# Performance work log

Hardware: AMD Instinct MI355X
Metric: run time of the kernel (lower is better)

The kernel has to match this reference:

```python
import jax, jax.numpy as jnp
import numpy as np

B, L, H = 16, 512, 1024
K_START, K_END = 5, 5
LN_EPS = 1e-12
NEG = 1e30


def _layer_norm(x, gamma, beta):
    mu = jnp.mean(x, axis=-1, keepdims=True)
    var = jnp.mean(jnp.square(x - mu), axis=-1, keepdims=True)
    return (x - mu) * jax.lax.rsqrt(var + LN_EPS) * gamma + beta


def setup_inputs() -> dict:
    key = jax.random.key(0)
    ks = jax.random.split(key, 10)
    s = 0.02
    sequence_data = jax.random.normal(ks[0], (B, L, H), jnp.float32)
    class_index = jax.random.randint(ks[1], (B,), 0, L, dtype=jnp.int32)
    paragraph_mask = (jax.random.uniform(ks[2], (B, L)) > 0.1).astype(jnp.float32)
    paragraph_mask = paragraph_mask.at[:, 0].set(1.0)  # guarantee >=1 valid position per row
    return {
        'sequence_data': sequence_data,
        'class_index': class_index,
        'paragraph_mask': paragraph_mask,
        'W_start': jax.random.normal(ks[3], (H, 1), jnp.float32) * s,
        'b_start': jnp.zeros((1,), jnp.float32),
        'W_end_in': jax.random.normal(ks[4], (2 * H, H), jnp.float32) * s,
        'b_end_in': jnp.zeros((H,), jnp.float32),
        'ln_gamma': jnp.ones((H,), jnp.float32),
        'ln_beta': jnp.zeros((H,), jnp.float32),
        'W_end_out': jax.random.normal(ks[5], (H, 1), jnp.float32) * s,
        'b_end_out': jnp.zeros((1,), jnp.float32),
        'W_ans_in': jax.random.normal(ks[6], (2 * H, H), jnp.float32) * s,
        'b_ans_in': jnp.zeros((H,), jnp.float32),
        'W_ans_out': jax.random.normal(ks[7], (H, 1), jnp.float32) * s,
    }


def reference(sequence_data, class_index, paragraph_mask,
              W_start, b_start, W_end_in, b_end_in, ln_gamma, ln_beta,
              W_end_out, b_end_out, W_ans_in, b_ans_in, W_ans_out):
    mask = paragraph_mask  # [b, l] float, 1 = valid

    # ---- start logits ----
    start_logits = jnp.einsum('blh,ho->bl', sequence_data, W_start) + b_start[0]  # [b,l]
    masked_start_logits = start_logits * mask - NEG * (1.0 - mask)
    start_predictions = jax.nn.log_softmax(masked_start_logits, axis=-1)

    # ---- beam search over start positions (inference branch) ----
    start_top_predictions, start_top_index = jax.lax.top_k(start_predictions, K_START)  # [b,k]
    # one-hot einsum gather 'blh,bkl->bkh' expressed as direct indexing
    start_features = jnp.take_along_axis(sequence_data, start_top_index[:, :, None], axis=1)  # [b,k,h]

    # end_logits inner dense on concat([tiled seq, tiled start_features]) along h:
    # split the [2h, h] kernel and broadcast-add instead of materializing the tiled concat.
    W1, W2 = W_end_in[:H], W_end_in[H:]
    inner = jnp.tanh(
        jnp.einsum('blh,hd->bld', sequence_data, W1)[:, :, None, :]
        + jnp.einsum('bkh,hd->bkd', start_features, W2)[:, None, :, :]
        + b_end_in
    )  # [b,l,k,h]
    inner = _layer_norm(inner, ln_gamma, ln_beta)
    end_logits = jnp.einsum('blkh,ho->blk', inner, W_end_out) + b_end_out[0]  # [b,l,k]
    end_logits = jnp.transpose(end_logits, (0, 2, 1))  # [b,k,l]

    mask_k = mask[:, None, :]  # [b,1,l]
    masked_end_logits = end_logits * mask_k - NEG * (1.0 - mask_k)
    end_predictions = jax.nn.log_softmax(masked_end_logits, axis=-1)

    end_top_predictions, _end_top_index = jax.lax.top_k(end_predictions, K_END)  # [b,k,k2]
    end_top_predictions = end_top_predictions.reshape(-1, K_START * K_END)

    # ---- answer (class) logits ----
    class_feature = sequence_data[jnp.arange(sequence_data.shape[0]), class_index]  # [b,h]
    start_p = jax.nn.softmax(masked_start_logits, axis=-1)
    start_feature = jnp.einsum('blh,bl->bh', sequence_data, start_p)
    answer_feature = jnp.concatenate([start_feature, class_feature], axis=-1)  # [b,2h]
    answer_feature = jnp.tanh(answer_feature @ W_ans_in + b_ans_in)  # dropout is identity at inference
    class_logits = (answer_feature @ W_ans_out)[:, 0]  # [b]

    return (start_predictions, end_predictions, masked_start_logits, masked_end_logits,
            start_top_predictions, end_top_predictions, class_logits)
```

## Files before the change

kernel.cpp:

```cpp
#include <hip/hip_runtime.h>
#include <math.h>

#define HD   1024
#define LSEQ 512
#define NB   16
#define KTOP 5
#define NEGV 1e30f

typedef __bf16 bf16x8 __attribute__((ext_vector_type(8)));
typedef float  f32x4  __attribute__((ext_vector_type(4)));

__device__ inline unsigned short f2bf(float f) {
  unsigned u = __float_as_uint(f);
  unsigned r = (u + 0x7FFFu + ((u >> 16) & 1u)) >> 16;
  return (unsigned short)r;
}
__device__ inline float bf2f(unsigned short u) {
  return __uint_as_float(((unsigned)u) << 16);
}

__device__ inline float fast_tanh(float x) {
  float e = __expf(-2.f * fabsf(x));
  float v = (1.f - e) / (1.f + e);
  return copysignf(v, x);
}

__device__ inline float tanh_scaled(float xs) {
  float e = __builtin_amdgcn_exp2f(xs);
  float r = __builtin_amdgcn_rcpf(1.f + e);
  return fmaf(-2.f, r, 1.f);
}

#define GLDS(g, l) __builtin_amdgcn_global_load_lds(                      \
    (const __attribute__((address_space(1))) unsigned int*)(g),          \
    (__attribute__((address_space(3))) unsigned int*)(l), 16, 0, 0)


__device__ __forceinline__ void sm_body(int row, const float* __restrict__ xin,
                                        float* __restrict__ lsm_out,
                                        float* __restrict__ top_out,
                                        float* __restrict__ p_out,
                                        int* __restrict__ idx_out) {
  __shared__ float redf[4];
  __shared__ int redi[4];
  __shared__ float bc_m, bc_s;
  __shared__ int bc_i;
  int t = threadIdx.x, lane = t & 63, wid = t >> 6;
  const float* x = xin + (size_t)row * LSEQ;
  float x0 = x[t], x1 = x[t + 256];

  float m = fmaxf(x0, x1);
#pragma unroll
  for (int off = 32; off; off >>= 1) m = fmaxf(m, __shfl_xor(m, off));
  if (lane == 0) redf[wid] = m;
  __syncthreads();
  if (t == 0) bc_m = fmaxf(fmaxf(redf[0], redf[1]), fmaxf(redf[2], redf[3]));
  __syncthreads();
  m = bc_m;

  float e0 = expf(x0 - m), e1 = expf(x1 - m);
  float s = e0 + e1;
#pragma unroll
  for (int off = 32; off; off >>= 1) s += __shfl_xor(s, off);
  if (lane == 0) redf[wid] = s;
  __syncthreads();
  if (t == 0) bc_s = redf[0] + redf[1] + redf[2] + redf[3];
  __syncthreads();
  s = bc_s;
  float ls = logf(s);

  lsm_out[(size_t)row * LSEQ + t] = x0 - m - ls;
  lsm_out[(size_t)row * LSEQ + t + 256] = x1 - m - ls;
  if (p_out) {
    float inv = 1.f / s;
    p_out[(size_t)row * LSEQ + t] = e0 * inv;
    p_out[(size_t)row * LSEQ + t + 256] = e1 * inv;
  }

  bool a0 = true, a1 = true;
  for (int it = 0; it < KTOP; ++it) {
    float v0 = a0 ? x0 : -INFINITY;
    float v1 = a1 ? x1 : -INFINITY;
    float bv = v0; int bi = t;
    if (v1 > bv) { bv = v1; bi = t + 256; }
#pragma unroll
    for (int off = 32; off; off >>= 1) {
      float ov = __shfl_xor(bv, off);
      int oi = __shfl_xor(bi, off);
      if (ov > bv || (ov == bv && oi < bi)) { bv = ov; bi = oi; }
    }
    __syncthreads();
    if (lane == 0) { redf[wid] = bv; redi[wid] = bi; }
    __syncthreads();
    if (t == 0) {
      float wv = redf[0]; int wi = redi[0];
      for (int w = 1; w < 4; ++w)
        if (redf[w] > wv || (redf[w] == wv && redi[w] < wi)) { wv = redf[w]; wi = redi[w]; }
      top_out[row * KTOP + it] = wv - m - ls;
      if (idx_out) idx_out[row * KTOP + it] = wi;
      bc_i = wi;
    }
    __syncthreads();
    int wi = bc_i;
    if (wi == t) a0 = false;
    if (wi == t + 256) a1 = false;
  }
}

__device__ __forceinline__ void gemm_body(int R0, int C0,
                                          const unsigned short* __restrict__ Abf,
                                          const unsigned short* __restrict__ Bt,
                                          unsigned short* __restrict__ X1) {
  __shared__ unsigned short SH[32768];
  unsigned short* As = SH;
  unsigned short* Bs = SH + 16384;
  int t = threadIdx.x;
  int w = t >> 6, lane = t & 63, ln = lane & 15, hi = lane >> 4;
  int wr = w >> 1, wc = w & 1;

  f32x4 acc[4][4] = {};

#define STAGE(buf, kc)                                                        \
  do {                                                                        \
    _Pragma("unroll")                                                         \
    for (int p_ = 0; p_ < 4; ++p_) {                                          \
      int rr_ = p_ * 32 + (t >> 3);                                           \
      int cc_ = (t & 7) ^ (rr_ & 7);                                          \
      GLDS(Abf + (size_t)(R0 + rr_) * HD + (kc) + cc_ * 8,                    \
           As + (buf) * 8192 + p_ * 2048 + w * 512);                          \
      GLDS(Bt + (size_t)(C0 + rr_) * HD + (kc) + cc_ * 8,                     \
           Bs + (buf) * 8192 + p_ * 2048 + w * 512);                          \
    }                                                                         \
  } while (0)

  STAGE(0, 0);
  for (int it = 0; it < 16; ++it) {
    int cur = it & 1;
    if (it < 15) {
      STAGE(cur ^ 1, (it + 1) * 64);
      asm volatile("s_waitcnt vmcnt(8)" ::: "memory");
    } else {
      asm volatile("s_waitcnt vmcnt(0)" ::: "memory");
    }
    __builtin_amdgcn_s_barrier();
    __builtin_amdgcn_sched_barrier(0);
#pragma unroll
    for (int ks = 0; ks < 2; ++ks) {
      bf16x8 av[4], bv[4];
#pragma unroll
      for (int m = 0; m < 4; ++m) {
        int r = wr * 64 + m * 16 + ln;
        av[m] = *(const bf16x8*)(const void*)&As[cur * 8192 + r * 64 + (((ks * 4 + hi) ^ (r & 7)) * 8)];
      }
#pragma unroll
      for (int n = 0; n < 4; ++n) {
        int r = wc * 64 + n * 16 + ln;
        bv[n] = *(const bf16x8*)(const void*)&Bs[cur * 8192 + r * 64 + (((ks * 4 + hi) ^ (r & 7)) * 8)];
      }
#pragma unroll
      for (int m = 0; m < 4; ++m)
#pragma unroll
        for (int n = 0; n < 4; ++n)
          acc[m][n] = __builtin_amdgcn_mfma_f32_16x16x32_bf16(av[m], bv[n], acc[m][n], 0, 0, 0);
    }
    __builtin_amdgcn_sched_barrier(0);
    __builtin_amdgcn_s_barrier();
  }
#undef STAGE

#pragma unroll
  for (int m = 0; m < 4; ++m)
#pragma unroll
    for (int j = 0; j < 4; ++j) {
      int row = R0 + wr * 64 + m * 16 + hi * 4 + j;
#pragma unroll
      for (int n = 0; n < 4; ++n) {
        int col = C0 + wc * 64 + n * 16 + ln;
        X1[(size_t)row * HD + col] = f2bf(acc[m][n][j]);
      }
    }
}

__device__ __forceinline__ void x2gemm_body(int cid,
                                            const unsigned short* __restrict__ seqb,
                                            const unsigned short* __restrict__ w2t,
                                            const int* __restrict__ idx,
                                            const float* __restrict__ bei,
                                            float* __restrict__ x2p) {
  __shared__ unsigned short SH2[32768];
  unsigned short* As = SH2;
  unsigned short* Bs = SH2 + 16384;
  int t = threadIdx.x;
  int w = t >> 6, lane = t & 63, ln = lane & 15, hi = lane >> 4;
  int wr = w >> 1, wc = w & 1;
  int C0 = cid * 128;

  size_t abase[4];
#pragma unroll
  for (int p_ = 0; p_ < 4; ++p_) {
    int rr = p_ * 32 + (t >> 3);
    int bk = rr < 80 ? rr : 0;
    int l = idx[bk];
    abase[p_] = ((size_t)((bk / KTOP) * LSEQ + l)) * HD;
  }

  f32x4 acc[4][4] = {};

#define STAGE2(buf, kc)                                                       \
  do {                                                                        \
    _Pragma("unroll")                                                         \
    for (int p_ = 0; p_ < 4; ++p_) {                                          \
      int rr_ = p_ * 32 + (t >> 3);                                           \
      int cc_ = (t & 7) ^ (rr_ & 7);                                          \
      GLDS(seqb + abase[p_] + (kc) + cc_ * 8,                                 \
           As + (buf) * 8192 + p_ * 2048 + w * 512);                          \
      GLDS(w2t + (size_t)(C0 + rr_) * HD + (kc) + cc_ * 8,                    \
           Bs + (buf) * 8192 + p_ * 2048 + w * 512);                          \
    }                                                                         \
  } while (0)

  STAGE2(0, 0);
  for (int it = 0; it < 16; ++it) {
    int cur = it & 1;
    if (it < 15) {
      STAGE2(cur ^ 1, (it + 1) * 64);
      asm volatile("s_waitcnt vmcnt(8)" ::: "memory");
    } else {
      asm volatile("s_waitcnt vmcnt(0)" ::: "memory");
    }
    __builtin_amdgcn_s_barrier();
    __builtin_amdgcn_sched_barrier(0);
#pragma unroll
    for (int ks = 0; ks < 2; ++ks) {
      bf16x8 av[4], bv[4];
#pragma unroll
      for (int m = 0; m < 4; ++m) {
        int r = wr * 64 + m * 16 + ln;
        av[m] = *(const bf16x8*)(const void*)&As[cur * 8192 + r * 64 + (((ks * 4 + hi) ^ (r & 7)) * 8)];
      }
#pragma unroll
      for (int n = 0; n < 4; ++n) {
        int r = wc * 64 + n * 16 + ln;
        bv[n] = *(const bf16x8*)(const void*)&Bs[cur * 8192 + r * 64 + (((ks * 4 + hi) ^ (r & 7)) * 8)];
      }
#pragma unroll
      for (int m = 0; m < 4; ++m)
#pragma unroll
        for (int n = 0; n < 4; ++n)
          acc[m][n] = __builtin_amdgcn_mfma_f32_16x16x32_bf16(av[m], bv[n], acc[m][n], 0, 0, 0);
    }
    __builtin_amdgcn_sched_barrier(0);
    __builtin_amdgcn_s_barrier();
  }
#undef STAGE2

#pragma unroll
  for (int m = 0; m < 4; ++m)
#pragma unroll
    for (int j = 0; j < 4; ++j) {
      int row = wr * 64 + m * 16 + hi * 4 + j;
      if (row < 80) {
#pragma unroll
        for (int n = 0; n < 4; ++n) {
          int col = C0 + wc * 64 + n * 16 + ln;
          x2p[(size_t)row * HD + col] = acc[m][n][j] + bei[col];
        }
      }
    }
}

__device__ __forceinline__ void ansin_body(int q, const float* __restrict__ seq,
                                           const float* __restrict__ p_ws,
                                           const int* __restrict__ cls,
                                           float* __restrict__ pa,
                                           float* __restrict__ cf) {
  __shared__ float ps[16];
  int b = q >> 5, s = q & 31, t = threadIdx.x;
  if (t < 16) ps[t] = p_ws[b * LSEQ + s * 16 + t];
  __syncthreads();
  const float* sb = seq + (size_t)(b * LSEQ + s * 16) * HD;
  float4 acc = make_float4(0.f, 0.f, 0.f, 0.f);
#pragma unroll
  for (int r = 0; r < 16; ++r) {
    float4 v = *(const float4*)(sb + (size_t)r * HD + 4 * t);
    float p = ps[r];
    acc.x = fmaf(p, v.x, acc.x);
    acc.y = fmaf(p, v.y, acc.y);
    acc.z = fmaf(p, v.z, acc.z);
    acc.w = fmaf(p, v.w, acc.w);
  }
  *(float4*)(pa + ((size_t)b * 32 + s) * HD + 4 * t) = acc;
  if (s == 0) {
    int ci = cls[b];
    *(float4*)(cf + (size_t)b * HD + 4 * t) =
        *(const float4*)(seq + (size_t)(b * LSEQ + ci) * HD + 4 * t);
  }
}

__device__ __forceinline__ void endrow_body(int bx, const unsigned short* __restrict__ X1,
                                            const float* __restrict__ x2p,
                                            const float* __restrict__ gw_ws,
                                            const float* __restrict__ sgb_ws,
                                            const float* __restrict__ mask,
                                            float* __restrict__ mel) {
  __shared__ float x2s[KTOP * HD];
  const float A = 2.885390081777927f;
  int t = threadIdx.x, wave = t >> 6, lane = t & 63;
  int row = bx * 4 + wave;
  int b = row >> 9, l = row & 511;

  {
    const float4* src = (const float4*)(x2p + (size_t)b * KTOP * HD);
    float4* dst = (float4*)x2s;
    for (int i = t; i < KTOP * HD / 4; i += 256) {
      float4 v = src[i];
      dst[i] = make_float4(v.x * A, v.y * A, v.z * A, v.w * A);
    }
  }

  float xs[16], gwr[16];
  const unsigned short* xrow = X1 + (size_t)row * HD + lane * 4;
#pragma unroll
  for (int q = 0; q < 4; ++q) {
    ushort4 u = *(const ushort4*)(xrow + q * 256);
    xs[4 * q + 0] = bf2f(u.x) * A;
    xs[4 * q + 1] = bf2f(u.y) * A;
    xs[4 * q + 2] = bf2f(u.z) * A;
    xs[4 * q + 3] = bf2f(u.w) * A;
    float4 g = *(const float4*)(gw_ws + q * 256 + lane * 4);
    gwr[4 * q + 0] = g.x; gwr[4 * q + 1] = g.y;
    gwr[4 * q + 2] = g.z; gwr[4 * q + 3] = g.w;
  }
  float mv = mask[row];
  float sG = sgb_ws[0], sBW = sgb_ws[1];
  __syncthreads();

#pragma unroll
  for (int k = 0; k < KTOP; ++k) {
    float sv = 0.f, s2 = 0.f, sg = 0.f;
#pragma unroll
    for (int q = 0; q < 4; ++q) {
      float4 xq = *(const float4*)&x2s[k * HD + q * 256 + lane * 4];
      float v0 = tanh_scaled(xs[4 * q + 0] + xq.x);
      float v1 = tanh_scaled(xs[4 * q + 1] + xq.y);
      float v2 = tanh_scaled(xs[4 * q + 2] + xq.z);
      float v3 = tanh_scaled(xs[4 * q + 3] + xq.w);
      sv += v0 + v1 + v2 + v3;
      s2 = fmaf(v0, v0, s2); s2 = fmaf(v1, v1, s2);
      s2 = fmaf(v2, v2, s2); s2 = fmaf(v3, v3, s2);
      sg = fmaf(v0, gwr[4 * q + 0], sg); sg = fmaf(v1, gwr[4 * q + 1], sg);
      sg = fmaf(v2, gwr[4 * q + 2], sg); sg = fmaf(v3, gwr[4 * q + 3], sg);
    }
#pragma unroll
    for (int off = 32; off; off >>= 1) {
      sv += __shfl_xor(sv, off);
      s2 += __shfl_xor(s2, off);
      sg += __shfl_xor(sg, off);
    }
    if (lane == 0) {
      float mu = sv * (1.f / (float)HD);
      float var = s2 * (1.f / (float)HD) - mu * mu;
      float rr = rsqrtf(var + 1e-12f);
      float logit = rr * (sg - mu * sG) + sBW;
      mel[((size_t)b * KTOP + k) * LSEQ + l] = logit * mv - NEGV * (1.f - mv);
    }
  }
}

__device__ __forceinline__ void ansmid_body(int q, const float* __restrict__ pa,
                                            const float* __restrict__ cf,
                                            const float* __restrict__ Wai,
                                            float* __restrict__ pans) {
  __shared__ float a_s[128];
  int b = q >> 4, c = q & 15, t = threadIdx.x;
  if (t < 128) {
    int i = c * 128 + t;
    float av;
    if (i < HD) {
      av = 0.f;
#pragma unroll
      for (int s = 0; s < 32; ++s) av += pa[((size_t)b * 32 + s) * HD + i];
    } else {
      av = cf[(size_t)b * HD + (i - HD)];
    }
    a_s[t] = av;
  }
  __syncthreads();
  float4 acc = make_float4(0.f, 0.f, 0.f, 0.f);
#pragma unroll 8
  for (int r = 0; r < 128; ++r) {
    float4 wv = *(const float4*)(Wai + (size_t)(c * 128 + r) * HD + 4 * t);
    float a = a_s[r];
    acc.x = fmaf(a, wv.x, acc.x);
    acc.y = fmaf(a, wv.y, acc.y);
    acc.z = fmaf(a, wv.z, acc.z);
    acc.w = fmaf(a, wv.w, acc.w);
  }
  *(float4*)(pans + ((size_t)b * 16 + c) * HD + 4 * t) = acc;
}

__device__ __forceinline__ void ansfinal_body(int b, const float* __restrict__ pans,
                                              const float* __restrict__ bai,
                                              const float* __restrict__ Wao,
                                              float* __restrict__ out6) {
  __shared__ float red[4];
  int t = threadIdx.x, lane = t & 63, wid = t >> 6;
  float4 a = *(const float4*)(bai + 4 * t);
#pragma unroll
  for (int c = 0; c < 16; ++c) {
    float4 p = *(const float4*)(pans + ((size_t)b * 16 + c) * HD + 4 * t);
    a.x += p.x; a.y += p.y; a.z += p.z; a.w += p.w;
  }
  float4 wo = *(const float4*)(Wao + 4 * t);
  float part = fast_tanh(a.x) * wo.x + fast_tanh(a.y) * wo.y +
               fast_tanh(a.z) * wo.z + fast_tanh(a.w) * wo.w;
#pragma unroll
  for (int off = 32; off; off >>= 1) part += __shfl_xor(part, off);
  if (lane == 0) red[wid] = part;
  __syncthreads();
  if (t == 0) out6[b] = red[0] + red[1] + red[2] + red[3];
}


__global__ void k_prep(const float* __restrict__ seq,
                       unsigned short* __restrict__ seqb,
                       const float* __restrict__ Wst,
                       const float* __restrict__ bst,
                       const float* __restrict__ mask,
                       float* __restrict__ msl,
                       const float* __restrict__ Wei,
                       unsigned short* __restrict__ w1t,
                       unsigned short* __restrict__ w2t,
                       const float* __restrict__ gam,
                       const float* __restrict__ bet,
                       const float* __restrict__ Weo,
                       const float* __restrict__ beo,
                       float* __restrict__ gw_ws,
                       float* __restrict__ sgb_ws) {
  __shared__ unsigned short tile[32][33];
  __shared__ float redp[4][2];
  int bx = blockIdx.x;
  if (bx < 2048) {
    int wave = threadIdx.x >> 6, lane = threadIdx.x & 63;
    int row = bx * 4 + wave;
    const float4* s4 = (const float4*)(seq + (size_t)row * HD);
    const float4* w4 = (const float4*)Wst;
    ushort4* o4 = (ushort4*)(seqb + (size_t)row * HD);
    float acc = 0.f;
#pragma unroll
    for (int m = 0; m < 4; ++m) {
      int i = lane + 64 * m;
      float4 a = s4[i], w = w4[i];
      acc += a.x * w.x + a.y * w.y + a.z * w.z + a.w * w.w;
      ushort4 o;
      o.x = f2bf(a.x); o.y = f2bf(a.y); o.z = f2bf(a.z); o.w = f2bf(a.w);
      o4[i] = o;
    }
#pragma unroll
    for (int off = 32; off; off >>= 1) acc += __shfl_xor(acc, off);
    if (lane == 0) {
      float logit = acc + bst[0];
      float mv = mask[row];
      msl[row] = logit * mv - NEGV * (1.f - mv);
    }
  } else if (bx < 4096) {
    int tb = bx - 2048;
    const float* Wsrc = Wei + (tb >= 1024 ? (size_t)HD * HD : 0);
    unsigned short* Wdst = (tb >= 1024) ? w2t : w1t;
    int tb2 = tb & 1023;
    int h0 = (tb2 & 31) * 32, d0 = (tb2 >> 5) * 32;
    int tx = threadIdx.x & 31, ty = threadIdx.x >> 5;
#pragma unroll
    for (int i = 0; i < 4; ++i)
      tile[ty + 8 * i][tx] = f2bf(Wsrc[(size_t)(h0 + ty + 8 * i) * HD + d0 + tx]);
    __syncthreads();
#pragma unroll
    for (int i = 0; i < 4; ++i)
      Wdst[(size_t)(d0 + ty + 8 * i) * HD + h0 + tx] = tile[tx][ty + 8 * i];
  } else {
    int t = threadIdx.x, wave = t >> 6, lane = t & 63;
    float4 g = ((const float4*)gam)[t];
    float4 w = ((const float4*)Weo)[t];
    float4 bv = ((const float4*)bet)[t];
    float4 gwv = make_float4(g.x * w.x, g.y * w.y, g.z * w.z, g.w * w.w);
    ((float4*)gw_ws)[t] = gwv;
    float pg = gwv.x + gwv.y + gwv.z + gwv.w;
    float pb = bv.x * w.x + bv.y * w.y + bv.z * w.z + bv.w * w.w;
#pragma unroll
    for (int off = 32; off; off >>= 1) {
      pg += __shfl_xor(pg, off);
      pb += __shfl_xor(pb, off);
    }
    if (lane == 0) { redp[wave][0] = pg; redp[wave][1] = pb; }
    __syncthreads();
    if (t == 0) {
      sgb_ws[0] = redp[0][0] + redp[1][0] + redp[2][0] + redp[3][0];
      sgb_ws[1] = redp[0][1] + redp[1][1] + redp[2][1] + redp[3][1] + beo[0];
    }
  }
}

__global__ void k_softmax_topk(const float* __restrict__ xin,
                               float* __restrict__ lsm_out,
                               float* __restrict__ top_out,
                               float* __restrict__ p_out,
                               int* __restrict__ idx_out) {
  sm_body(blockIdx.x, xin, lsm_out, top_out, p_out, idx_out);
}

__launch_bounds__(256, 2)
__global__ void k_gsm(const unsigned short* __restrict__ Abf,
                      const unsigned short* __restrict__ Bt,
                      unsigned short* __restrict__ X1,
                      const float* __restrict__ msl,
                      float* __restrict__ lsm_out,
                      float* __restrict__ top_out,
                      float* __restrict__ p_out,
                      int* __restrict__ idx_out) {
  int id = blockIdx.x;
  if (id < 16) {
    sm_body(id, msl, lsm_out, top_out, p_out, idx_out);
  } else {
    int gid = id - 16;
    gemm_body((gid & 63) * 128, (gid >> 6) * 128, Abf, Bt, X1);
  }
}

__launch_bounds__(256, 2)
__global__ void k_x2a(const unsigned short* __restrict__ seqb,
                      const unsigned short* __restrict__ w2t,
                      const int* __restrict__ idx,
                      const float* __restrict__ bei,
                      float* __restrict__ x2p,
                      const float* __restrict__ seq,
                      const float* __restrict__ p_ws,
                      const int* __restrict__ cls,
                      float* __restrict__ pa,
                      float* __restrict__ cf) {
  int id = blockIdx.x;
  if (id < 8) x2gemm_body(id, seqb, w2t, idx, bei, x2p);
  else ansin_body(id - 8, seq, p_ws, cls, pa, cf);
}

__global__ void k_end2(const unsigned short* __restrict__ X1,
                       const float* __restrict__ x2p,
                       const float* __restrict__ gw_ws,
                       const float* __restrict__ sgb_ws,
                       const float* __restrict__ mask,
                       float* __restrict__ mel,
                       const float* __restrict__ pa,
                       const float* __restrict__ cf,
                       const float* __restrict__ Wai,
                       float* __restrict__ pans) {
  int bx = blockIdx.x;
  if (bx < 2048) endrow_body(bx, X1, x2p, gw_ws, sgb_ws, mask, mel);
  else ansmid_body(bx - 2048, pa, cf, Wai, pans);
}

__global__ void k_fin(const float* __restrict__ mel,
                      float* __restrict__ lsm_out,
                      float* __restrict__ top_out,
                      const float* __restrict__ pans,
                      const float* __restrict__ bai,
                      const float* __restrict__ Wao,
                      float* __restrict__ out6) {
  int bx = blockIdx.x;
  if (bx < NB * KTOP) sm_body(bx, mel, lsm_out, top_out, nullptr, nullptr);
  else ansfinal_body(bx - NB * KTOP, pans, bai, Wao, out6);
}

__global__ void k_x2init(const float* __restrict__ bei, float* __restrict__ x2p) {
  ((float4*)(x2p + (size_t)blockIdx.x * HD))[threadIdx.x] = ((const float4*)bei)[threadIdx.x];
}

__global__ void k_x2f(const float* __restrict__ seq, const int* __restrict__ idx,
                      const float* __restrict__ Wei, float* __restrict__ x2p) {
  __shared__ float srow[128];
  int q = blockIdx.x;
  int bk = q >> 3, s = q & 7, t = threadIdx.x;
  int b = bk / KTOP;
  int l = idx[bk];
  if (t < 128) srow[t] = seq[((size_t)(b * LSEQ + l)) * HD + s * 128 + t];
  __syncthreads();
  const float* W2 = Wei + (size_t)HD * HD + (size_t)s * 128 * HD;
  float4 acc = make_float4(0.f, 0.f, 0.f, 0.f);
#pragma unroll 8
  for (int h = 0; h < 128; ++h) {
    float4 wv = *(const float4*)(W2 + (size_t)h * HD + 4 * t);
    float sv = srow[h];
    acc.x = fmaf(sv, wv.x, acc.x);
    acc.y = fmaf(sv, wv.y, acc.y);
    acc.z = fmaf(sv, wv.z, acc.z);
    acc.w = fmaf(sv, wv.w, acc.w);
  }
  float* dst = x2p + (size_t)bk * HD + 4 * t;
  atomicAdd(dst + 0, acc.x);
  atomicAdd(dst + 1, acc.y);
  atomicAdd(dst + 2, acc.z);
  atomicAdd(dst + 3, acc.w);
}

__global__ void k_ansin_f(const float* __restrict__ seq, const float* __restrict__ p_ws,
                          const int* __restrict__ cls, float* __restrict__ pa,
                          float* __restrict__ cf) {
  ansin_body(blockIdx.x, seq, p_ws, cls, pa, cf);
}
__global__ void k_ansmid_f(const float* __restrict__ pa, const float* __restrict__ cf,
                           const float* __restrict__ Wai, float* __restrict__ pans) {
  ansmid_body(blockIdx.x, pa, cf, Wai, pans);
}

__launch_bounds__(256, 2)
__global__ void k_gemm_end_at(const unsigned short* __restrict__ Abf,
                              const unsigned short* __restrict__ Bt,
                              const float* __restrict__ x2p,
                              const float* __restrict__ gamma,
                              const float* __restrict__ Wout,
                              float* __restrict__ outp) {
  __shared__ unsigned short As[2][128 * 64];
  __shared__ unsigned short Bs[2][128 * 64];
  int t = threadIdx.x;
  int w = t >> 6, lane = t & 63, ln = lane & 15, hi = lane >> 4;
  int wr = w >> 1, wc = w & 1;
  int R0 = blockIdx.x * 128, C0 = blockIdx.y * 128;
  int b = R0 >> 9;
  f32x4 acc[4][4] = {};
#define STAGE(buf, kc)                                                        \
  do {                                                                        \
    _Pragma("unroll")                                                         \
    for (int p_ = 0; p_ < 4; ++p_) {                                          \
      int rr_ = p_ * 32 + (t >> 3);                                           \
      int cc_ = (t & 7) ^ (rr_ & 7);                                          \
      GLDS(Abf + (size_t)(R0 + rr_) * HD + (kc) + cc_ * 8,                    \
           &As[buf][p_ * 2048 + w * 512]);                                    \
      GLDS(Bt + (size_t)(C0 + rr_) * HD + (kc) + cc_ * 8,                     \
           &Bs[buf][p_ * 2048 + w * 512]);                                    \
    }                                                                         \
  } while (0)
  STAGE(0, 0);
  for (int it = 0; it < 16; ++it) {
    int cur = it & 1;
    if (it < 15) {
      STAGE(cur ^ 1, (it + 1) * 64);
      asm volatile("s_waitcnt vmcnt(8)" ::: "memory");
    } else {
      asm volatile("s_waitcnt vmcnt(0)" ::: "memory");
    }
    __builtin_amdgcn_s_barrier();
    __builtin_amdgcn_sched_barrier(0);
#pragma unroll
    for (int ks = 0; ks < 2; ++ks) {
      bf16x8 av[4], bv[4];
#pragma unroll
      for (int m = 0; m < 4; ++m) {
        int r = wr * 64 + m * 16 + ln;
        av[m] = *(const bf16x8*)(const void*)&As[cur][r * 64 + (((ks * 4 + hi) ^ (r & 7)) * 8)];
      }
#pragma unroll
      for (int n = 0; n < 4; ++n) {
        int r = wc * 64 + n * 16 + ln;
        bv[n] = *(const bf16x8*)(const void*)&Bs[cur][r * 64 + (((ks * 4 + hi) ^ (r & 7)) * 8)];
      }
#pragma unroll
      for (int m = 0; m < 4; ++m)
#pragma unroll
        for (int n = 0; n < 4; ++n)
          acc[m][n] = __builtin_amdgcn_mfma_f32_16x16x32_bf16(av[m], bv[n], acc[m][n], 0, 0, 0);
    }
    __builtin_amdgcn_sched_barrier(0);
    __builtin_amdgcn_s_barrier();
  }
#undef STAGE
  float gsv[4];
  float x2v[4][KTOP];
#pragma unroll
  for (int n = 0; n < 4; ++n) {
    int c = C0 + wc * 64 + n * 16 + ln;
    gsv[n] = gamma[c] * Wout[c];
#pragma unroll
    for (int k = 0; k < KTOP; ++k) x2v[n][k] = x2p[((size_t)b * KTOP + k) * HD + c];
  }
#pragma unroll
  for (int m = 0; m < 4; ++m)
#pragma unroll
    for (int j = 0; j < 4; ++j) {
      int row = R0 + wr * 64 + m * 16 + hi * 4 + j;
#pragma unroll
      for (int k = 0; k < KTOP; ++k) {
        float sv = 0.f, s2 = 0.f, sg = 0.f;
#pragma unroll
        for (int n = 0; n < 4; ++n) {
          float v = fast_tanh(acc[m][n][j] + x2v[n][k]);
          sv += v; s2 += v * v; sg += v * gsv[n];
        }
#pragma unroll
        for (int off = 8; off; off >>= 1) {
          sv += __shfl_xor(sv, off);
          s2 += __shfl_xor(s2, off);
          sg += __shfl_xor(sg, off);
        }
        if (ln == 0) {
          float* p = outp + ((size_t)row * KTOP + k) * 3;
          atomicAdd(p, sv);
          atomicAdd(p + 1, s2);
          atomicAdd(p + 2, sg);
        }
      }
    }
}

__global__ void k_end_final(const float* __restrict__ sums,
                            const float* __restrict__ gamma,
                            const float* __restrict__ beta,
                            const float* __restrict__ Wout,
                            const float* __restrict__ beo,
                            const float* __restrict__ mask,
                            float* __restrict__ mel) {
  int bk = blockIdx.x, b = bk / KTOP, k = bk % KTOP;
  int t = threadIdx.x, lane = t & 63, wid = t >> 6;
  __shared__ float red[4][2];
  float pg = 0.f, pb = 0.f;
  for (int i = t; i < HD; i += 256) {
    float wv = Wout[i];
    pg += gamma[i] * wv;
    pb += beta[i] * wv;
  }
#pragma unroll
  for (int off = 32; off; off >>= 1) {
    pg += __shfl_xor(pg, off);
    pb += __shfl_xor(pb, off);
  }
  if (lane == 0) { red[wid][0] = pg; red[wid][1] = pb; }
  __syncthreads();
  float sG = red[0][0] + red[1][0] + red[2][0] + red[3][0];
  float sBW = red[0][1] + red[1][1] + red[2][1] + red[3][1] + beo[0];
  for (int l = t; l < LSEQ; l += 256) {
    int row = b * LSEQ + l;
    const float* s = sums + ((size_t)row * KTOP + k) * 3;
    float sv = s[0], s2 = s[1], sg = s[2];
    float mu = sv * (1.f / (float)HD);
    float var = s2 * (1.f / (float)HD) - mu * mu;
    float rr = rsqrtf(var + 1e-12f);
    float logit = rr * (sg - mu * sG) + sBW;
    float mv = mask[row];
    mel[((size_t)b * KTOP + k) * LSEQ + l] = logit * mv - NEGV * (1.f - mv);
  }
}

extern "C" void kernel_launch(void* const* d_in, const int* in_sizes, int n_in,
                              void* d_out, int out_size, void* d_ws, size_t ws_size,
                              hipStream_t stream) {
  (void)in_sizes; (void)n_in; (void)out_size;
  const float* seq = (const float*)d_in[0];
  const int*   cls = (const int*)d_in[1];
  const float* mask = (const float*)d_in[2];
  const float* Wst = (const float*)d_in[3];
  const float* bst = (const float*)d_in[4];
  const float* Wei = (const float*)d_in[5];
  const float* bei = (const float*)d_in[6];
  const float* gam = (const float*)d_in[7];
  const float* bet = (const float*)d_in[8];
  const float* Weo = (const float*)d_in[9];
  const float* beo = (const float*)d_in[10];
  const float* Wai = (const float*)d_in[11];
  const float* bai = (const float*)d_in[12];
  const float* Wao = (const float*)d_in[13];

  float* out = (float*)d_out;
  float* out0 = out;
  float* out1 = out0 + 8192;
  float* out2 = out1 + 40960;
  float* out3 = out2 + 8192;
  float* out4 = out3 + 40960;
  float* out5 = out4 + 80;
  float* out6 = out5 + 400;

  char* p = (char*)d_ws;
  unsigned short* seqb = (unsigned short*)p;  p += (size_t)8192 * 1024 * 2;
  unsigned short* w1t  = (unsigned short*)p;  p += (size_t)1024 * 1024 * 2;
  unsigned short* w2t  = (unsigned short*)p;  p += (size_t)1024 * 1024 * 2;
  float* p_ws   = (float*)p;                  p += 8192 * 4;
  int*   idx_ws = (int*)p;                    p += 128 * 4;
  float* x2p    = (float*)p;                  p += (size_t)80 * 1024 * 4;
  float* gw_ws  = (float*)p;                  p += 1024 * 4;
  float* sgb_ws = (float*)p;                  p += 4 * 4;
  float* pa     = (float*)p;                  p += (size_t)16 * 32 * 1024 * 4;
  float* cf     = (float*)p;                  p += (size_t)16 * 1024 * 4;
  float* pans   = (float*)p;                  p += (size_t)16 * 16 * 1024 * 4;
  unsigned short* x1 = (unsigned short*)p;
  float* sums = (float*)p;
  size_t base = (size_t)(p - (char*)d_ws);
  size_t need_big = base + (size_t)8192 * 1024 * 2;
  size_t need_small = base + (size_t)8192 * KTOP * 3 * 4;

  k_prep<<<4097, 256, 0, stream>>>(seq, seqb, Wst, bst, mask, out2, Wei, w1t, w2t,
                                   gam, bet, Weo, beo, gw_ws, sgb_ws);

  if (ws_size >= need_big) {
    k_gsm<<<528, 256, 0, stream>>>(seqb, w1t, x1, out2, out0, out4, p_ws, idx_ws);
    k_x2a<<<520, 256, 0, stream>>>(seqb, w2t, idx_ws, bei, x2p,
                                   seq, p_ws, cls, pa, cf);
    k_end2<<<2304, 256, 0, stream>>>(x1, x2p, gw_ws, sgb_ws, mask, out3,
                                     pa, cf, Wai, pans);
  } else if (ws_size >= need_small) {
    k_softmax_topk<<<NB, 256, 0, stream>>>(out2, out0, out4, p_ws, idx_ws);
    k_x2init<<<80, 256, 0, stream>>>(bei, x2p);
    k_x2f<<<640, 256, 0, stream>>>(seq, idx_ws, Wei, x2p);
    hipMemsetAsync(sums, 0, (size_t)8192 * KTOP * 3 * sizeof(float), stream);
    k_gemm_end_at<<<dim3(64, 8), 256, 0, stream>>>(seqb, w1t, x2p, gam, Weo, sums);
    k_end_final<<<NB * KTOP, 256, 0, stream>>>(sums, gam, bet, Weo, beo, mask, out3);
    k_ansin_f<<<512, 256, 0, stream>>>(seq, p_ws, cls, pa, cf);
    k_ansmid_f<<<256, 256, 0, stream>>>(pa, cf, Wai, pans);
  }

  k_fin<<<96, 256, 0, stream>>>(out3, out1, out5, pans, bai, Wao, out6);
}
```

Measured before the change: 88.71 us.

## Fold softmax-weighted answer pooling into GEMM launch with interleaved block scheduling

Each answer-pooling block now recomputes the row softmax of the masked start logits itself, so the pooling no longer depends on the softmax blocks. That lets it move into the first GEMM launch, interleaved with the GEMM tiles in groups of 8. The second launch then only runs the small 8-block x2 GEMM, which shortens the critical path between kernels. The cost is redundant per-block softmax reductions and 1056 blocks, some of which are idle padding; sm_body is now called with a null p_out pointer, which it must tolerate.

```diff
diff --git a/kernel.cpp b/kernel.cpp
--- a/kernel.cpp
+++ b/kernel.cpp
@@ -267,6 +267,57 @@
         }
       }
     }
+}
+
+__device__ __forceinline__ void ansin_ms_body(int q, const float* __restrict__ seq,
+                                              const float* __restrict__ msl,
+                                              const int* __restrict__ cls,
+                                              float* __restrict__ pa,
+                                              float* __restrict__ cf) {
+  __shared__ float ared[4];
+  __shared__ float a_m, a_s;
+  __shared__ float ps[16];
+  int b = q >> 5, sl = q & 31, t = threadIdx.x;
+  int lane = t & 63, wid = t >> 6;
+
+  const float* x = msl + (size_t)b * LSEQ;
+  float x0 = x[t], x1 = x[t + 256];
+  float m = fmaxf(x0, x1);
+#pragma unroll
+  for (int off = 32; off; off >>= 1) m = fmaxf(m, __shfl_xor(m, off));
+  if (lane == 0) ared[wid] = m;
+  __syncthreads();
+  if (t == 0) a_m = fmaxf(fmaxf(ared[0], ared[1]), fmaxf(ared[2], ared[3]));
+  __syncthreads();
+  m = a_m;
+  float e = expf(x0 - m) + expf(x1 - m);
+#pragma unroll
+  for (int off = 32; off; off >>= 1) e += __shfl_xor(e, off);
+  if (lane == 0) ared[wid] = e;
+  __syncthreads();
+  if (t == 0) a_s = ared[0] + ared[1] + ared[2] + ared[3];
+  __syncthreads();
+  float inv = 1.f / a_s;
+  if (t < 16) ps[t] = expf(x[sl * 16 + t] - m) * inv;
+  __syncthreads();
+
+  const float* sb = seq + (size_t)(b * LSEQ + sl * 16) * HD;
+  float4 acc = make_float4(0.f, 0.f, 0.f, 0.f);
+#pragma unroll
+  for (int r = 0; r < 16; ++r) {
+    float4 v = *(const float4*)(sb + (size_t)r * HD + 4 * t);
+    float p = ps[r];
+    acc.x = fmaf(p, v.x, acc.x);
+    acc.y = fmaf(p, v.y, acc.y);
+    acc.z = fmaf(p, v.z, acc.z);
+    acc.w = fmaf(p, v.w, acc.w);
+  }
+  *(float4*)(pa + ((size_t)b * 32 + sl) * HD + 4 * t) = acc;
+  if (sl == 0) {
+    int ci = cls[b];
+    *(float4*)(cf + (size_t)b * HD + 4 * t) =
+        *(const float4*)(seq + (size_t)(b * LSEQ + ci) * HD + 4 * t);
+  }
 }
 
 __device__ __forceinline__ void ansin_body(int q, const float* __restrict__ seq,
@@ -515,31 +566,30 @@
                       const float* __restrict__ msl,
                       float* __restrict__ lsm_out,
                       float* __restrict__ top_out,
-                      float* __restrict__ p_out,
-                      int* __restrict__ idx_out) {
-  int id = blockIdx.x;
-  if (id < 16) {
-    sm_body(id, msl, lsm_out, top_out, p_out, idx_out);
-  } else {
-    int gid = id - 16;
-    gemm_body((gid & 63) * 128, (gid >> 6) * 128, Abf, Bt, X1);
-  }
-}
-
-__launch_bounds__(256, 2)
-__global__ void k_x2a(const unsigned short* __restrict__ seqb,
-                      const unsigned short* __restrict__ w2t,
-                      const int* __restrict__ idx,
-                      const float* __restrict__ bei,
-                      float* __restrict__ x2p,
+                      int* __restrict__ idx_out,
                       const float* __restrict__ seq,
-                      const float* __restrict__ p_ws,
                       const int* __restrict__ cls,
                       float* __restrict__ pa,
                       float* __restrict__ cf) {
   int id = blockIdx.x;
-  if (id < 8) x2gemm_body(id, seqb, w2t, idx, bei, x2p);
-  else ansin_body(id - 8, seq, p_ws, cls, pa, cf);
+  int grp = id >> 4, j = id & 15;
+  if (j < 8) {
+    int g = grp * 8 + j;
+    if (g < 512) gemm_body((g & 63) * 128, (g >> 6) * 128, Abf, Bt, X1);
+  } else {
+    int o = grp * 8 + (j - 8);
+    if (o < 16) sm_body(o, msl, lsm_out, top_out, nullptr, idx_out);
+    else if (o < 528) ansin_ms_body(o - 16, seq, msl, cls, pa, cf);
+  }
+}
+
+__launch_bounds__(256, 2)
+__global__ void k_x2g(const unsigned short* __restrict__ seqb,
+                      const unsigned short* __restrict__ w2t,
+                      const int* __restrict__ idx,
+                      const float* __restrict__ bei,
+                      float* __restrict__ x2p) {
+  x2gemm_body(blockIdx.x, seqb, w2t, idx, bei, x2p);
 }
 
 __global__ void k_end2(const unsigned short* __restrict__ X1,
@@ -797,9 +847,9 @@
                                    gam, bet, Weo, beo, gw_ws, sgb_ws);
 
   if (ws_size >= need_big) {
-    k_gsm<<<528, 256, 0, stream>>>(seqb, w1t, x1, out2, out0, out4, p_ws, idx_ws);
-    k_x2a<<<520, 256, 0, stream>>>(seqb, w2t, idx_ws, bei, x2p,
-                                   seq, p_ws, cls, pa, cf);
+    k_gsm<<<1056, 256, 0, stream>>>(seqb, w1t, x1, out2, out0, out4, idx_ws,
+                                    seq, cls, pa, cf);
+    k_x2g<<<8, 256, 0, stream>>>(seqb, w2t, idx_ws, bei, x2p);
     k_end2<<<2304, 256, 0, stream>>>(x1, x2p, gw_ws, sgb_ws, mask, out3,
                                      pa, cf, Wai, pans);
   } else if (ws_size >= need_small) {
```

After: 94.25 us. 1.06x slower.

## Replace double-buffered GEMM staging with single buffer to raise occupancy

Applied to the files above, without the earlier changes.

Both bf16 MFMA GEMM bodies drop their LDS double buffering. They now load each K-chunk, wait for it fully, compute, then synchronize before the next load. Shared memory per block halves and launch bounds go from 2 to 4 blocks per CU, aiming to hide latency through more resident waves instead of in-block prefetch. The trade-off is that load and compute no longer overlap within a block, and a tighter register cap may cause spills.

```diff
diff --git a/kernel.cpp b/kernel.cpp
--- a/kernel.cpp
+++ b/kernel.cpp
@@ -111,51 +111,45 @@
                                           const unsigned short* __restrict__ Abf,
                                           const unsigned short* __restrict__ Bt,
                                           unsigned short* __restrict__ X1) {
-  __shared__ unsigned short SH[32768];
+  __shared__ unsigned short SH[16384];
   unsigned short* As = SH;
-  unsigned short* Bs = SH + 16384;
+  unsigned short* Bs = SH + 8192;
   int t = threadIdx.x;
   int w = t >> 6, lane = t & 63, ln = lane & 15, hi = lane >> 4;
   int wr = w >> 1, wc = w & 1;
 
   f32x4 acc[4][4] = {};
 
-#define STAGE(buf, kc)                                                        \
+#define STAGE(kc)                                                             \
   do {                                                                        \
     _Pragma("unroll")                                                         \
     for (int p_ = 0; p_ < 4; ++p_) {                                          \
       int rr_ = p_ * 32 + (t >> 3);                                           \
       int cc_ = (t & 7) ^ (rr_ & 7);                                          \
       GLDS(Abf + (size_t)(R0 + rr_) * HD + (kc) + cc_ * 8,                    \
-           As + (buf) * 8192 + p_ * 2048 + w * 512);                          \
+           As + p_ * 2048 + w * 512);                                         \
       GLDS(Bt + (size_t)(C0 + rr_) * HD + (kc) + cc_ * 8,                     \
-           Bs + (buf) * 8192 + p_ * 2048 + w * 512);                          \
+           Bs + p_ * 2048 + w * 512);                                         \
     }                                                                         \
   } while (0)
 
-  STAGE(0, 0);
   for (int it = 0; it < 16; ++it) {
-    int cur = it & 1;
-    if (it < 15) {
-      STAGE(cur ^ 1, (it + 1) * 64);
-      asm volatile("s_waitcnt vmcnt(8)" ::: "memory");
-    } else {
-      asm volatile("s_waitcnt vmcnt(0)" ::: "memory");
-    }
+    if (it) __syncthreads();
+    STAGE(it * 64);
+    asm volatile("s_waitcnt vmcnt(0)" ::: "memory");
     __builtin_amdgcn_s_barrier();
-    __builtin_amdgcn_sched_barrier(0);
 #pragma unroll
     for (int ks = 0; ks < 2; ++ks) {
       bf16x8 av[4], bv[4];
 #pragma unroll
       for (int m = 0; m < 4; ++m) {
         int r = wr * 64 + m * 16 + ln;
-        av[m] = *(const bf16x8*)(const void*)&As[cur * 8192 + r * 64 + (((ks * 4 + hi) ^ (r & 7)) * 8)];
+        av[m] = *(const bf16x8*)(const void*)&As[r * 64 + (((ks * 4 + hi) ^ (r & 7)) * 8)];
       }
 #pragma unroll
       for (int n = 0; n < 4; ++n) {
         int r = wc * 64 + n * 16 + ln;
-        bv[n] = *(const bf16x8*)(const void*)&Bs[cur * 8192 + r * 64 + (((ks * 4 + hi) ^ (r & 7)) * 8)];
+        bv[n] = *(const bf16x8*)(const void*)&Bs[r * 64 + (((ks * 4 + hi) ^ (r & 7)) * 8)];
       }
 #pragma unroll
       for (int m = 0; m < 4; ++m)
@@ -163,8 +157,6 @@
         for (int n = 0; n < 4; ++n)
           acc[m][n] = __builtin_amdgcn_mfma_f32_16x16x32_bf16(av[m], bv[n], acc[m][n], 0, 0, 0);
     }
-    __builtin_amdgcn_sched_barrier(0);
-    __builtin_amdgcn_s_barrier();
   }
 #undef STAGE
 
@@ -187,9 +179,9 @@
                                             const int* __restrict__ idx,
                                             const float* __restrict__ bei,
                                             float* __restrict__ x2p) {
-  __shared__ unsigned short SH2[32768];
+  __shared__ unsigned short SH2[16384];
   unsigned short* As = SH2;
-  unsigned short* Bs = SH2 + 16384;
+  unsigned short* Bs = SH2 + 8192;
   int t = threadIdx.x;
   int w = t >> 6, lane = t & 63, ln = lane & 15, hi = lane >> 4;
   int wr = w >> 1, wc = w & 1;
@@ -206,42 +198,36 @@
 
   f32x4 acc[4][4] = {};
 
-#define STAGE2(buf, kc)                                                       \
+#define STAGE2(kc)                                                            \
   do {                                                                        \
     _Pragma("unroll")                                                         \
     for (int p_ = 0; p_ < 4; ++p_) {                                          \
       int rr_ = p_ * 32 + (t >> 3);                                           \
       int cc_ = (t & 7) ^ (rr_ & 7);                                          \
       GLDS(seqb + abase[p_] + (kc) + cc_ * 8,                                 \
-           As + (buf) * 8192 + p_ * 2048 + w * 512);                          \
+           As + p_ * 2048 + w * 512);                                         \
       GLDS(w2t + (size_t)(C0 + rr_) * HD + (kc) + cc_ * 8,                    \
-           Bs + (buf) * 8192 + p_ * 2048 + w * 512);                          \
+           Bs + p_ * 2048 + w * 512);                                         \
     }                                                                         \
   } while (0)
 
-  STAGE2(0, 0);
   for (int it = 0; it < 16; ++it) {
-    int cur = it & 1;
-    if (it < 15) {
-      STAGE2(cur ^ 1, (it + 1) * 64);
-      asm volatile("s_waitcnt vmcnt(8)" ::: "memory");
-    } else {
-      asm volatile("s_waitcnt vmcnt(0)" ::: "memory");
-    }
+    if (it) __syncthreads();
+    STAGE2(it * 64);
+    asm volatile("s_waitcnt vmcnt(0)" ::: "memory");
     __builtin_amdgcn_s_barrier();
-    __builtin_amdgcn_sched_barrier(0);
 #pragma unroll
     for (int ks = 0; ks < 2; ++ks) {
       bf16x8 av[4], bv[4];
 #pragma unroll
       for (int m = 0; m < 4; ++m) {
         int r = wr * 64 + m * 16 + ln;
-        av[m] = *(const bf16x8*)(const void*)&As[cur * 8192 + r * 64 + (((ks * 4 + hi) ^ (r & 7)) * 8)];
+        av[m] = *(const bf16x8*)(const void*)&As[r * 64 + (((ks * 4 + hi) ^ (r & 7)) * 8)];
       }
 #pragma unroll
       for (int n = 0; n < 4; ++n) {
         int r = wc * 64 + n * 16 + ln;
-        bv[n] = *(const bf16x8*)(const void*)&Bs[cur * 8192 + r * 64 + (((ks * 4 + hi) ^ (r & 7)) * 8)];
+        bv[n] = *(const bf16x8*)(const void*)&Bs[r * 64 + (((ks * 4 + hi) ^ (r & 7)) * 8)];
       }
 #pragma unroll
       for (int m = 0; m < 4; ++m)
@@ -249,8 +235,6 @@
         for (int n = 0; n < 4; ++n)
           acc[m][n] = __builtin_amdgcn_mfma_f32_16x16x32_bf16(av[m], bv[n], acc[m][n], 0, 0, 0);
     }
-    __builtin_amdgcn_sched_barrier(0);
-    __builtin_amdgcn_s_barrier();
   }
 #undef STAGE2
 
@@ -508,7 +492,7 @@
   sm_body(blockIdx.x, xin, lsm_out, top_out, p_out, idx_out);
 }
 
-__launch_bounds__(256, 2)
+__launch_bounds__(256, 4)
 __global__ void k_gsm(const unsigned short* __restrict__ Abf,
                       const unsigned short* __restrict__ Bt,
                       unsigned short* __restrict__ X1,
@@ -526,7 +510,7 @@
   }
 }
 
-__launch_bounds__(256, 2)
+__launch_bounds__(256, 4)
 __global__ void k_x2a(const unsigned short* __restrict__ seqb,
                       const unsigned short* __restrict__ w2t,
                       const int* __restrict__ idx,
```

After: 87.92 us. About the same (-0.9%).
